# Kernel tuning notes

Measured on AMD Instinct MI355X. Metric: run time of the kernel, lower is better.

## Reference

```python
import jax, jax.numpy as jnp
import numpy as np
from jax import lax

HEADS = 8
WIN_SIZES = (2, 4, 8)


def _linear(x, w, b):
    return x @ w + b


def _window_attention(x2d, ws, w4, b4):
    # x2d: (B,H,W,C); w4: (4,C,C) = [q,k,v,out]; b4: (4,C)
    B, H, W, C = x2d.shape
    p1, p2 = H // ws, W // ws
    xw = x2d.reshape(B, p1, ws, p2, ws, C).transpose(0, 1, 3, 2, 4, 5)
    xw = xw.reshape(B, p1, p2, ws * ws, C)
    hs = C // HEADS
    q = _linear(xw, w4[0], b4[0]).reshape(B, p1, p2, ws * ws, HEADS, hs)
    k = _linear(xw, w4[1], b4[1]).reshape(B, p1, p2, ws * ws, HEADS, hs)
    v = _linear(xw, w4[2], b4[2]).reshape(B, p1, p2, ws * ws, HEADS, hs)
    scores = jnp.einsum('bpqwhd,bpqvhd->bpqhwv', q, k) / jnp.sqrt(jnp.asarray(hs, x2d.dtype))
    probs = jax.nn.softmax(scores, axis=-1)
    ctx = jnp.einsum('bpqhwv,bpqvhd->bpqwhd', probs, v).reshape(B, p1, p2, ws * ws, C)
    return _linear(ctx, w4[3], b4[3])


def _unwindow(out, ws):
    B, p1, p2, win, C = out.shape
    s = out.reshape(B, p1, p2, ws, ws, C).transpose(0, 1, 3, 2, 4, 5)
    return s.reshape(B, p1 * ws, p2 * ws, C)


def _up_bilinear_ac(x, oh, ow):
    # x: (B,C,h,w); bilinear with align_corners=True (UpsamplingBilinear2d)
    B, C, h, w = x.shape
    def grid(o, i):
        pos = jnp.arange(o, dtype=x.dtype) * ((i - 1) / (o - 1))
        i0 = jnp.floor(pos).astype(jnp.int32)
        i1 = jnp.minimum(i0 + 1, i - 1)
        return i0, i1, pos - i0.astype(x.dtype)
    r0, r1, tr = grid(oh, h)
    c0, c1, tc = grid(ow, w)
    xr = x[:, :, r0, :] * (1 - tr)[None, None, :, None] + x[:, :, r1, :] * tr[None, None, :, None]
    return xr[:, :, :, c0] * (1 - tc) + xr[:, :, :, c1] * tc


def _forward(x, attn_w, attn_b, edge_w, mlp_w1, mlp_b1, mlp_w2, mlp_b2,
             dl_w, dl_b, ax_w, ax_b, g_shift, g_bias, sq_w, sq_b):
    B, N, C = x.shape
    H = W = int(np.sqrt(N))
    x2d = x.reshape(B, H, W, C)

    # multi-scale window attention branches
    scale_outputs = [_unwindow(_window_attention(x2d, ws, attn_w[i], attn_b[i]), ws)
                     for i, ws in enumerate(WIN_SIZES)]

    # adaptive window selector
    xc = x2d.transpose(0, 3, 1, 2)  # (B,C,H,W)
    edge = jnp.abs(lax.conv_general_dilated(xc, edge_w, (1, 1), 'SAME'))
    avg = lax.reduce_window(edge, 0.0, lax.add, (1, 1, 3, 3), (1, 1, 1, 1), 'SAME') / 9.0
    e = avg.transpose(0, 2, 3, 1)  # (B,H,W,1)
    wts = jax.nn.softmax(jax.nn.relu(e @ mlp_w1 + mlp_b1) @ mlp_w2 + mlp_b2, axis=-1)

    blended = sum(wts[..., i:i + 1] * scale_outputs[i] for i in range(len(WIN_SIZES)))
    h_map = blended.transpose(0, 3, 1, 2)  # (B,C,H,W)

    # ws=4 window attention -> DlightConv token pooling
    x_win = _window_attention(x2d, 4, attn_w[1], attn_b[1])  # (B,p,p,16,C)
    probs = jax.nn.softmax(jnp.mean(x_win, axis=-2) @ dl_w + dl_b, axis=-1)
    x_dl = jnp.sum(x_win * probs[..., None], axis=-2)  # (B,p,p,C)

    # axial attention (no head split, no scaling in the axial branch)
    q = _linear(x_dl, ax_w[0], ax_b[0])
    k = _linear(x_dl, ax_w[1], ax_b[1])
    v = _linear(x_dl, ax_w[2], ax_b[2])
    scores_x = jnp.einsum('bhwc,bhvc->bhwv', q, k)  # (B,r,c,k)
    scores_y = jnp.einsum('bhwc,bvwc->bwhv', q, k)  # (B,c,r,k)

    # GaussianTrans: vectorized per-pixel gaussian positional bias
    p = x_dl.shape[1]
    idx = jnp.arange(p, dtype=x.dtype)
    dist2 = (idx[None, :] - idx[:, None]) ** 2          # [pos, k]
    gb = -(g_shift[0] * dist2 + g_bias[0])              # (p,p)
    ax = jax.nn.softmax(scores_x + gb[None, None, :, :], axis=-1)       # bias indexed by c
    ay = jax.nn.softmax(jnp.swapaxes(scores_y, 1, 2) + gb[None, :, None, :], axis=-1)  # bias by r
    x_g = jnp.einsum('brck,brkd->brcd', ax, v) + jnp.einsum('brck,bkcd->brcd', ay, v)

    x_g = _up_bilinear_ac(x_g.transpose(0, 3, 1, 2), H, W)  # (B,C,H,W)

    cat = jnp.concatenate([x_g, h_map], axis=1)  # (B,2C,H,W)
    out = jnp.einsum('oc,bchw->bohw', sq_w, cat) + sq_b[None, :, None, None]
    return out.transpose(0, 2, 3, 1).reshape(B, N, C)


def setup_inputs() -> dict:
    key = jax.random.key(0)
    ks = jax.random.split(key, 16)
    B, N, C = 16, 4096, 256
    s = 0.02
    return {
        'x': jax.random.normal(ks[0], (B, N, C), jnp.float32),
        'attn_w': jax.random.normal(ks[1], (3, 4, C, C), jnp.float32) * s,
        'attn_b': jax.random.normal(ks[2], (3, 4, C), jnp.float32) * s,
        'edge_w': jax.random.normal(ks[3], (1, C, 3, 3), jnp.float32) * s,
        'mlp_w1': jax.random.normal(ks[4], (1, 16), jnp.float32) * s,
        'mlp_b1': jax.random.normal(ks[5], (16,), jnp.float32) * s,
        'mlp_w2': jax.random.normal(ks[6], (16, 3), jnp.float32) * s,
        'mlp_b2': jax.random.normal(ks[7], (3,), jnp.float32) * s,
        'dl_w': jax.random.normal(ks[8], (C, 16), jnp.float32) * s,
        'dl_b': jax.random.normal(ks[9], (16,), jnp.float32) * s,
        'ax_w': jax.random.normal(ks[10], (3, C, C), jnp.float32) * s,
        'ax_b': jax.random.normal(ks[11], (3, C), jnp.float32) * s,
        'g_shift': jnp.abs(jax.random.normal(ks[12], (1,), jnp.float32)),
        'g_bias': -jnp.abs(jax.random.normal(ks[13], (1,), jnp.float32)),
        'sq_w': jax.random.normal(ks[14], (C, 2 * C), jnp.float32) * s,
        'sq_b': jax.random.normal(ks[15], (C,), jnp.float32) * s,
    }


def reference(x, attn_w, attn_b, edge_w, mlp_w1, mlp_b1, mlp_w2, mlp_b2,
              dl_w, dl_b, ax_w, ax_b, g_shift, g_bias, sq_w, sq_b):
    return _forward(x, attn_w, attn_b, edge_w, mlp_w1, mlp_b1, mlp_w2, mlp_b2,
                    dl_w, dl_b, ax_w, ax_b, g_shift, g_bias, sq_w, sq_b)
```

## Files before the change

kernel.cpp:

```cpp
#include <hip/hip_runtime.h>
#include <math.h>


#define CHUNK_B 4
#define CHUNK_TOK (CHUNK_B * 4096)
#define KS 32

typedef __attribute__((ext_vector_type(8))) short short8;
typedef __attribute__((ext_vector_type(8))) unsigned short ushort8;
typedef __attribute__((ext_vector_type(4))) float f32x4;

__device__ __forceinline__ ushort f2bf(float f) {
    union { float f; unsigned u; } v; v.f = f;
    unsigned r = v.u + 0x7fff + ((v.u >> 16) & 1);
    return (ushort)(r >> 16);
}
__device__ __forceinline__ float bf2f(ushort h) {
    union { unsigned u; float f; } v; v.u = ((unsigned)h) << 16; return v.f;
}
__device__ __forceinline__ void split2(float v, ushort& h, ushort& l) {
    h = f2bf(v);
    l = f2bf(v - bf2f(h));
}

__global__ __launch_bounds__(256) void split_w_kmajor(
    const float* __restrict__ W, ushort* __restrict__ Th, ushort* __restrict__ Tl, int nmats)
{
    const int idx = blockIdx.x * 256 + threadIdx.x;
    if (idx >= nmats * 65536) return;
    const int mat = idx >> 16, r = idx & 65535;
    const int n = r >> 8, k = r & 255;
    const float v = W[(size_t)mat * 65536 + k * 256 + n];
    ushort h, l; split2(v, h, l);
    Th[idx] = h; Tl[idx] = l;
}
__global__ __launch_bounds__(256) void split_w_nmajor(
    const float* __restrict__ W, ushort* __restrict__ Th, ushort* __restrict__ Tl, int total)
{
    const int idx = blockIdx.x * 256 + threadIdx.x;
    if (idx >= total) return;
    ushort h, l; split2(W[idx], h, l);
    Th[idx] = h; Tl[idx] = l;
}

__global__ __launch_bounds__(256) void split_x(
    const float* __restrict__ X, ushort* __restrict__ Xh, ushort* __restrict__ Xl)
{
    const size_t i4 = (size_t)blockIdx.x * 256 + threadIdx.x;
    const float4 v = *(const float4*)(X + i4 * 4);
    ushort4 h, l;
    split2(v.x, h.x, l.x); split2(v.y, h.y, l.y);
    split2(v.z, h.z, l.z); split2(v.w, h.w, l.w);
    *(ushort4*)(Xh + i4 * 4) = h;
    *(ushort4*)(Xl + i4 * 4) = l;
}

#define GEMM_DECLS                                                            \
    __shared__ ushort Ah[128 * KS], Al[128 * KS], Bh[128 * KS], Bl[128 * KS]; \
    const int tid = threadIdx.x;                                              \
    const int wave = tid >> 6, lane = tid & 63;                               \
    const int quad = lane >> 4, l16 = lane & 15;                              \
    const int wr = (wave >> 1) * 64, wc = (wave & 1) * 64;                    \
    f32x4 acc[4][4];                                                          \
    _Pragma("unroll") for (int i = 0; i < 4; i++)                             \
        _Pragma("unroll") for (int j = 0; j < 4; j++)                         \
            acc[i][j] = (f32x4){0.f, 0.f, 0.f, 0.f};

#define STAGE_US(dst, src, strideE, rowbase, k0e)                             \
    _Pragma("unroll") for (int cc = 0; cc < 2; cc++) {                        \
        const int ch = tid + cc * 256;                                        \
        const int r = ch >> 2, kc = (ch & 3) * 8;                             \
        *(ushort8*)&(dst)[ch * 8] =                                           \
            *(const ushort8*)((src) + (size_t)((rowbase) + r) * (strideE) + (k0e) + kc); \
    }

#define STAGE_F32(AhD, AlD, Aptr, kk)                                         \
    _Pragma("unroll") for (int cc = 0; cc < 2; cc++) {                        \
        const int ch = tid + cc * 256;                                        \
        const int r = ch >> 2, kc = (ch & 3) * 8;                             \
        const float* p = (Aptr) + (size_t)(m0 + r) * 256 + (kk) + kc;         \
        const float4 v0 = *(const float4*)p;                                  \
        const float4 v1 = *(const float4*)(p + 4);                            \
        ushort8 h, l; ushort hh, ll;                                          \
        split2(v0.x, hh, ll); h[0] = hh; l[0] = ll;                           \
        split2(v0.y, hh, ll); h[1] = hh; l[1] = ll;                           \
        split2(v0.z, hh, ll); h[2] = hh; l[2] = ll;                           \
        split2(v0.w, hh, ll); h[3] = hh; l[3] = ll;                           \
        split2(v1.x, hh, ll); h[4] = hh; l[4] = ll;                           \
        split2(v1.y, hh, ll); h[5] = hh; l[5] = ll;                           \
        split2(v1.z, hh, ll); h[6] = hh; l[6] = ll;                           \
        split2(v1.w, hh, ll); h[7] = hh; l[7] = ll;                           \
        *(ushort8*)&(AhD)[ch * 8] = h;                                        \
        *(ushort8*)&(AlD)[ch * 8] = l;                                        \
    }

#define GEMM_COMPUTE                                                          \
    {                                                                         \
        short8 afh[4], afl[4], bfh[4], bfl[4];                                \
        _Pragma("unroll") for (int i = 0; i < 4; i++) {                       \
            const int ro = (wr + i * 16 + l16) * KS + quad * 8;               \
            afh[i] = *(const short8*)&Ah[ro];                                 \
            afl[i] = *(const short8*)&Al[ro];                                 \
        }                                                                     \
        _Pragma("unroll") for (int j = 0; j < 4; j++) {                       \
            const int no = (wc + j * 16 + l16) * KS + quad * 8;               \
            bfh[j] = *(const short8*)&Bh[no];                                 \
            bfl[j] = *(const short8*)&Bl[no];                                 \
        }                                                                     \
        _Pragma("unroll") for (int i = 0; i < 4; i++)                         \
            _Pragma("unroll") for (int j = 0; j < 4; j++) {                   \
                acc[i][j] = __builtin_amdgcn_mfma_f32_16x16x32_bf16(          \
                    afh[i], bfh[j], acc[i][j], 0, 0, 0);                      \
                acc[i][j] = __builtin_amdgcn_mfma_f32_16x16x32_bf16(          \
                    afl[i], bfh[j], acc[i][j], 0, 0, 0);                      \
                acc[i][j] = __builtin_amdgcn_mfma_f32_16x16x32_bf16(          \
                    afh[i], bfl[j], acc[i][j], 0, 0, 0);                      \
            }                                                                 \
    }

__global__ __launch_bounds__(256, 2) void gemm3_mfma(
    const ushort* __restrict__ AgH, const ushort* __restrict__ AgL,
    const ushort* __restrict__ Wth, const ushort* __restrict__ Wtl,
    const float* __restrict__ b0, const float* __restrict__ b1, const float* __restrict__ b2,
    float* __restrict__ O0, float* __restrict__ O1, float* __restrict__ O2)
{
    const int m0 = blockIdx.x * 128;
    const int mat = blockIdx.y >> 1;
    const int col0 = (blockIdx.y & 1) * 128;
    const ushort* wth = Wth + (size_t)mat * 65536 + (size_t)col0 * 256;
    const ushort* wtl = Wtl + (size_t)mat * 65536 + (size_t)col0 * 256;
    GEMM_DECLS
    for (int k0 = 0; k0 < 256; k0 += 32) {
        STAGE_US(Ah, AgH, 256, m0, k0)
        STAGE_US(Al, AgL, 256, m0, k0)
        STAGE_US(Bh, wth, 256, 0, k0)
        STAGE_US(Bl, wtl, 256, 0, k0)
        __syncthreads();
        GEMM_COMPUTE
        __syncthreads();
    }
    const float* bias = (mat == 0) ? b0 : (mat == 1) ? b1 : b2;
    float* O = (mat == 0) ? O0 : (mat == 1) ? O1 : O2;
#pragma unroll
    for (int j = 0; j < 4; j++) {
        const int col = col0 + wc + j * 16 + l16;
        const float bj = bias[col];
#pragma unroll
        for (int i = 0; i < 4; i++) {
            const int rbase = m0 + wr + i * 16 + quad * 4;
#pragma unroll
            for (int r = 0; r < 4; r++)
                O[(size_t)(rbase + r) * 256 + col] = acc[i][j][r] + bj;
        }
    }
}

__global__ __launch_bounds__(256, 2) void gemmp_mfma(
    const ushort* __restrict__ AgH, const ushort* __restrict__ AgL,
    const ushort* __restrict__ Wth, const ushort* __restrict__ Wtl,
    const float* __restrict__ bias,
    float* __restrict__ Sout, int store_s,
    float* __restrict__ Blnd, const float* __restrict__ wts, int scale_idx, int blend_init,
    int row_off)
{
    const int m0 = blockIdx.x * 128;
    const int col0 = blockIdx.y * 128;
    const ushort* wth = Wth + (size_t)col0 * 256;
    const ushort* wtl = Wtl + (size_t)col0 * 256;
    GEMM_DECLS
    for (int k0 = 0; k0 < 256; k0 += 32) {
        STAGE_US(Ah, AgH, 256, m0, k0)
        STAGE_US(Al, AgL, 256, m0, k0)
        STAGE_US(Bh, wth, 256, 0, k0)
        STAGE_US(Bl, wtl, 256, 0, k0)
        __syncthreads();
        GEMM_COMPUTE
        __syncthreads();
    }
#pragma unroll
    for (int i = 0; i < 4; i++) {
        const int rbase = m0 + wr + i * 16 + quad * 4;
#pragma unroll
        for (int r = 0; r < 4; r++) {
            const size_t grow = (size_t)row_off + rbase + r;
            const float wt = wts[grow * 3 + scale_idx];
#pragma unroll
            for (int j = 0; j < 4; j++) {
                const int col = col0 + wc + j * 16 + l16;
                const float v = acc[i][j][r] + bias[col];
                if (store_s) Sout[grow * 256 + col] = v;
                float* bp = Blnd + grow * 256 + col;
                if (blend_init) *bp = wt * v;
                else            *bp = *bp + wt * v;
            }
        }
    }
}

__global__ __launch_bounds__(256, 2) void gemmf_mfma(
    const ushort* __restrict__ UPH, const ushort* __restrict__ UPL,
    const float* __restrict__ BLD,
    const ushort* __restrict__ Wth, const ushort* __restrict__ Wtl,
    const float* __restrict__ SQB, float* __restrict__ OUT)
{
    const int m0 = blockIdx.x * 128;
    const int col0 = blockIdx.y * 128;
    const ushort* wth = Wth + (size_t)col0 * 512;
    const ushort* wtl = Wtl + (size_t)col0 * 512;
    GEMM_DECLS
    for (int k0 = 0; k0 < 512; k0 += 32) {
        if (k0 < 256) {
            STAGE_US(Ah, UPH, 256, m0, k0)
            STAGE_US(Al, UPL, 256, m0, k0)
        } else {
            STAGE_F32(Ah, Al, BLD, (k0 & 255))
        }
        STAGE_US(Bh, wth, 512, 0, k0)
        STAGE_US(Bl, wtl, 512, 0, k0)
        __syncthreads();
        GEMM_COMPUTE
        __syncthreads();
    }
#pragma unroll
    for (int j = 0; j < 4; j++) {
        const int col = col0 + wc + j * 16 + l16;
        const float bj = SQB[col];
#pragma unroll
        for (int i = 0; i < 4; i++) {
            const int rbase = m0 + wr + i * 16 + quad * 4;
#pragma unroll
            for (int r = 0; r < 4; r++)
                OUT[(size_t)(rbase + r) * 256 + col] = acc[i][j][r] + bj;
        }
    }
}

template <int WS, int NH>
__global__ __launch_bounds__(256) void win_attn(
    const float* __restrict__ Q, const float* __restrict__ K,
    const float* __restrict__ V, ushort* __restrict__ CTXh, ushort* __restrict__ CTXl)
{
    constexpr int WIN = WS * WS;
    constexpr int NW = 64 / WS;
    constexpr int CW = NH * 32;
    __shared__ float qs[WIN][CW + 4], ks[WIN][CW + 4], vs[WIN][CW + 4];
    __shared__ float sc[NH][WIN][WIN + 1];
    const int tid = threadIdx.x;
    const int wid = blockIdx.x;
    const int b = wid / (NW * NW);
    const int rem = wid % (NW * NW);
    const int p = rem / NW, q = rem % NW;
    const int h0 = blockIdx.y * NH;

    for (int idx = tid; idx < WIN * CW; idx += 256) {
        const int i = idx / CW;
        const int cc = idx % CW;
        const int ti = i / WS, tj = i % WS;
        const size_t g = ((size_t)(b * 4096 + (p * WS + ti) * 64 + (q * WS + tj))) * 256 + h0 * 32 + cc;
        qs[i][cc] = Q[g]; ks[i][cc] = K[g]; vs[i][cc] = V[g];
    }
    __syncthreads();
    const float scale = 0.17677669529663687f;
    for (int idx = tid; idx < NH * WIN * WIN; idx += 256) {
        const int hl = idx / (WIN * WIN);
        const int r = idx % (WIN * WIN);
        const int i = r / WIN, j = r % WIN;
        const int co = hl * 32;
        float s = 0.f;
#pragma unroll
        for (int d = 0; d < 32; d++) s += qs[i][co + d] * ks[j][co + d];
        sc[hl][i][j] = s * scale;
    }
    __syncthreads();
    if (tid < NH * WIN) {
        const int hl = tid / WIN, i = tid % WIN;
        float mx = -3.4e38f;
        for (int j = 0; j < WIN; j++) mx = fmaxf(mx, sc[hl][i][j]);
        float sum = 0.f;
        for (int j = 0; j < WIN; j++) {
            float e = __expf(sc[hl][i][j] - mx);
            sc[hl][i][j] = e; sum += e;
        }
        const float inv = 1.f / sum;
        for (int j = 0; j < WIN; j++) sc[hl][i][j] *= inv;
    }
    __syncthreads();
    for (int idx = tid; idx < WIN * CW; idx += 256) {
        const int i = idx / CW;
        const int cc = idx % CW;
        const int hl = cc >> 5;
        float s = 0.f;
        for (int j = 0; j < WIN; j++) s += sc[hl][i][j] * vs[j][cc];
        const int ti = i / WS, tj = i % WS;
        const size_t g = ((size_t)(b * 4096 + (p * WS + ti) * 64 + (q * WS + tj))) * 256 + h0 * 32 + cc;
        ushort hh, ll; split2(s, hh, ll);
        CTXh[g] = hh; CTXl[g] = ll;
    }
}

__global__ __launch_bounds__(256) void edge_gemm9(
    const float* __restrict__ x, const float* __restrict__ ew, float* __restrict__ ytmp)
{
    __shared__ float wsm[2304];
    const int tid = threadIdx.x;
    for (int i = tid; i < 2304; i += 256) wsm[i] = ew[i];
    __syncthreads();
    const int wave = tid >> 6, lane = tid & 63;
    const int p = blockIdx.x * 4 + wave;
    const float4 xv = *(const float4*)(x + (size_t)p * 256 + lane * 4);
    float acc[9];
#pragma unroll
    for (int t = 0; t < 9; t++) acc[t] = 0.f;
    const float xs[4] = {xv.x, xv.y, xv.z, xv.w};
#pragma unroll
    for (int i = 0; i < 4; i++) {
        const int c = lane * 4 + i;
#pragma unroll
        for (int t = 0; t < 9; t++)
            acc[t] = fmaf(xs[i], wsm[c * 9 + t], acc[t]);
    }
#pragma unroll
    for (int t = 0; t < 9; t++) {
#pragma unroll
        for (int off = 1; off < 64; off <<= 1)
            acc[t] += __shfl_xor(acc[t], off);
    }
    if (lane < 9) {
        float v = acc[0];
        switch (lane) {
            case 1: v = acc[1]; break; case 2: v = acc[2]; break;
            case 3: v = acc[3]; break; case 4: v = acc[4]; break;
            case 5: v = acc[5]; break; case 6: v = acc[6]; break;
            case 7: v = acc[7]; break; case 8: v = acc[8]; break;
            default: break;
        }
        ytmp[(size_t)p * 9 + lane] = v;
    }
}

__global__ __launch_bounds__(256) void edge_combine(
    const float* __restrict__ ytmp, float* __restrict__ edge)
{
    const int idx = blockIdx.x * 256 + threadIdx.x;
    const int b = idx >> 12, rem = idx & 4095, h = rem >> 6, w = rem & 63;
    float s = 0.f;
#pragma unroll
    for (int kh = 0; kh < 3; kh++) {
        const int hh = h + kh - 1;
        if ((unsigned)hh > 63u) continue;
#pragma unroll
        for (int kw = 0; kw < 3; kw++) {
            const int ww = w + kw - 1;
            if ((unsigned)ww > 63u) continue;
            s += ytmp[((size_t)b * 4096 + hh * 64 + ww) * 9 + kh * 3 + kw];
        }
    }
    edge[idx] = fabsf(s);
}

__global__ __launch_bounds__(256) void avg_mlp(
    const float* __restrict__ edge, const float* __restrict__ w1, const float* __restrict__ b1,
    const float* __restrict__ w2, const float* __restrict__ b2, float* __restrict__ wts)
{
    const int idx = blockIdx.x * 256 + threadIdx.x;
    const int b = idx >> 12, rem = idx & 4095, h = rem >> 6, w = rem & 63;
    float s = 0.f;
#pragma unroll
    for (int kh = -1; kh <= 1; kh++) {
        const int hh = h + kh;
        if ((unsigned)hh > 63u) continue;
#pragma unroll
        for (int kw = -1; kw <= 1; kw++) {
            const int ww = w + kw;
            if ((unsigned)ww > 63u) continue;
            s += edge[(size_t)b * 4096 + hh * 64 + ww];
        }
    }
    const float e = s / 9.f;
    float l0 = b2[0], l1 = b2[1], l2 = b2[2];
#pragma unroll
    for (int j = 0; j < 16; j++) {
        float hd = fmaxf(e * w1[j] + b1[j], 0.f);
        l0 += hd * w2[j * 3 + 0];
        l1 += hd * w2[j * 3 + 1];
        l2 += hd * w2[j * 3 + 2];
    }
    const float mx = fmaxf(l0, fmaxf(l1, l2));
    const float e0 = __expf(l0 - mx), e1 = __expf(l1 - mx), e2 = __expf(l2 - mx);
    const float inv = 1.f / (e0 + e1 + e2);
    wts[(size_t)idx * 3 + 0] = e0 * inv;
    wts[(size_t)idx * 3 + 1] = e1 * inv;
    wts[(size_t)idx * 3 + 2] = e2 * inv;
}

__global__ __launch_bounds__(256) void dlight(
    const float* __restrict__ S1, const float* __restrict__ dlw,
    const float* __restrict__ dlb, ushort* __restrict__ XDLH, ushort* __restrict__ XDLL)
{
    __shared__ float xw[16][257];
    __shared__ float m[256];
    __shared__ float pr[16];
    __shared__ float pr2[16];
    const int wid = blockIdx.x;
    const int b = wid >> 8, rem = wid & 255, p = rem >> 4, q = rem & 15;
    const int tid = threadIdx.x;
#pragma unroll
    for (int t = 0; t < 16; t++) {
        const int ti = t >> 2, tj = t & 3;
        xw[t][tid] = S1[((size_t)b * 4096 + (p * 4 + ti) * 64 + (q * 4 + tj)) * 256 + tid];
    }
    float mm = 0.f;
#pragma unroll
    for (int t = 0; t < 16; t++) mm += xw[t][tid];
    m[tid] = mm * (1.f / 16.f);
    __syncthreads();
    if (tid < 16) {
        float lg = dlb[tid];
        for (int c = 0; c < 256; c++) lg += m[c] * dlw[c * 16 + tid];
        pr[tid] = lg;
    }
    __syncthreads();
    if (tid < 16) {
        float mx = -3.4e38f;
        for (int j = 0; j < 16; j++) mx = fmaxf(mx, pr[j]);
        float sum = 0.f;
        for (int j = 0; j < 16; j++) sum += __expf(pr[j] - mx);
        pr2[tid] = __expf(pr[tid] - mx) / sum;
    }
    __syncthreads();
    float o = 0.f;
#pragma unroll
    for (int t = 0; t < 16; t++) o += xw[t][tid] * pr2[t];
    ushort hh, ll; split2(o, hh, ll);
    XDLH[(size_t)wid * 256 + tid] = hh;
    XDLL[(size_t)wid * 256 + tid] = ll;
}

__global__ __launch_bounds__(256) void axial_row(
    const float* __restrict__ Q, const float* __restrict__ K, const float* __restrict__ V,
    const float* __restrict__ gsp, const float* __restrict__ gbp, float* __restrict__ XG)
{
    __shared__ float qs[16][257], ks[16][257], vs[16][257];
    __shared__ float sc[16][17];
    const int bid = blockIdx.x;
    const int b = bid >> 4, r = bid & 15;
    const int tid = threadIdx.x;
    const float gs = gsp[0], gb = gbp[0];
#pragma unroll
    for (int w = 0; w < 16; w++) {
        const size_t base = ((size_t)b * 256 + r * 16 + w) * 256 + tid;
        qs[w][tid] = Q[base]; ks[w][tid] = K[base]; vs[w][tid] = V[base];
    }
    __syncthreads();
    {
        const int w = tid >> 4, vv = tid & 15;
        float s = 0.f;
        for (int c = 0; c < 256; c++) s += qs[w][c] * ks[vv][c];
        const float d = (float)(w - vv);
        sc[w][vv] = s - (gs * d * d + gb);
    }
    __syncthreads();
    if (tid < 16) {
        float mx = -3.4e38f;
        for (int j = 0; j < 16; j++) mx = fmaxf(mx, sc[tid][j]);
        float sum = 0.f;
        for (int j = 0; j < 16; j++) {
            float e = __expf(sc[tid][j] - mx);
            sc[tid][j] = e; sum += e;
        }
        const float inv = 1.f / sum;
        for (int j = 0; j < 16; j++) sc[tid][j] *= inv;
    }
    __syncthreads();
#pragma unroll
    for (int w2 = 0; w2 < 16; w2++) {
        float o = 0.f;
#pragma unroll
        for (int k2 = 0; k2 < 16; k2++) o += sc[w2][k2] * vs[k2][tid];
        XG[((size_t)b * 256 + r * 16 + w2) * 256 + tid] = o;
    }
}

__global__ __launch_bounds__(256) void axial_col(
    const float* __restrict__ Q, const float* __restrict__ K, const float* __restrict__ V,
    const float* __restrict__ gsp, const float* __restrict__ gbp, float* __restrict__ XG)
{
    __shared__ float qs[16][257], ks[16][257], vs[16][257];
    __shared__ float sc[16][17];
    const int bid = blockIdx.x;
    const int b = bid >> 4, col = bid & 15;
    const int tid = threadIdx.x;
    const float gs = gsp[0], gb = gbp[0];
#pragma unroll
    for (int h = 0; h < 16; h++) {
        const size_t base = ((size_t)b * 256 + h * 16 + col) * 256 + tid;
        qs[h][tid] = Q[base]; ks[h][tid] = K[base]; vs[h][tid] = V[base];
    }
    __syncthreads();
    {
        const int r = tid >> 4, vv = tid & 15;
        float s = 0.f;
        for (int c = 0; c < 256; c++) s += qs[r][c] * ks[vv][c];
        const float d = (float)(r - vv);
        sc[r][vv] = s - (gs * d * d + gb);
    }
    __syncthreads();
    if (tid < 16) {
        float mx = -3.4e38f;
        for (int j = 0; j < 16; j++) mx = fmaxf(mx, sc[tid][j]);
        float sum = 0.f;
        for (int j = 0; j < 16; j++) {
            float e = __expf(sc[tid][j] - mx);
            sc[tid][j] = e; sum += e;
        }
        const float inv = 1.f / sum;
        for (int j = 0; j < 16; j++) sc[tid][j] *= inv;
    }
    __syncthreads();
#pragma unroll
    for (int r2 = 0; r2 < 16; r2++) {
        float o = 0.f;
#pragma unroll
        for (int k2 = 0; k2 < 16; k2++) o += sc[r2][k2] * vs[k2][tid];
        XG[((size_t)b * 256 + r2 * 16 + col) * 256 + tid] += o;
    }
}

__global__ __launch_bounds__(256) void upsample(
    const float* __restrict__ XG, ushort* __restrict__ UPH, ushort* __restrict__ UPL)
{
    const unsigned idx = blockIdx.x * 256u + threadIdx.x;
    const int c = idx & 255;
    const unsigned t2 = idx >> 8;
    const int w = t2 & 63;
    const unsigned t3 = t2 >> 6;
    const int h = t3 & 63;
    const int b = t3 >> 6;
    const float rr = 15.f / 63.f;
    const float ph = h * rr, pw = w * rr;
    int h0 = (int)floorf(ph); float th = ph - (float)h0; int h1 = min(h0 + 1, 15);
    int w0 = (int)floorf(pw); float tw = pw - (float)w0; int w1 = min(w0 + 1, 15);
    const size_t bb = (size_t)b * 256;
    const float v00 = XG[((bb + h0 * 16 + w0)) * 256 + c];
    const float v10 = XG[((bb + h1 * 16 + w0)) * 256 + c];
    const float v01 = XG[((bb + h0 * 16 + w1)) * 256 + c];
    const float v11 = XG[((bb + h1 * 16 + w1)) * 256 + c];
    const float c0 = v00 * (1.f - th) + v10 * th;
    const float c1 = v01 * (1.f - th) + v11 * th;
    const float val = c0 * (1.f - tw) + c1 * tw;
    ushort hh, ll; split2(val, hh, ll);
    UPH[idx] = hh; UPL[idx] = ll;
}

extern "C" void kernel_launch(void* const* d_in, const int* in_sizes, int n_in,
                              void* d_out, int out_size, void* d_ws, size_t ws_size,
                              hipStream_t stream)
{
    const float* x      = (const float*)d_in[0];
    const float* attn_w = (const float*)d_in[1];
    const float* attn_b = (const float*)d_in[2];
    const float* edge_w = (const float*)d_in[3];
    const float* mlp_w1 = (const float*)d_in[4];
    const float* mlp_b1 = (const float*)d_in[5];
    const float* mlp_w2 = (const float*)d_in[6];
    const float* mlp_b2 = (const float*)d_in[7];
    const float* dl_w   = (const float*)d_in[8];
    const float* dl_b   = (const float*)d_in[9];
    const float* ax_w   = (const float*)d_in[10];
    const float* ax_b   = (const float*)d_in[11];
    const float* g_shift= (const float*)d_in[12];
    const float* g_bias = (const float*)d_in[13];
    const float* sq_w   = (const float*)d_in[14];
    const float* sq_b   = (const float*)d_in[15];
    float* out = (float*)d_out;

    float* ws = (float*)d_ws;
    const size_t MT = 65536;
    float* blend = ws;
    float* s1    = blend + MT * 256;
    float* scr   = s1 + MT * 256;
    float* chQ   = scr;
    float* chK   = chQ + (size_t)CHUNK_TOK * 256;
    float* chV   = chK + (size_t)CHUNK_TOK * 256;
    ushort* ctxh = (ushort*)(chV + (size_t)CHUNK_TOK * 256);
    ushort* ctxl = ctxh + (size_t)CHUNK_TOK * 256;
    ushort* uph  = (ushort*)scr;
    ushort* upl  = uph + MT * 256;
    float* ytmp  = scr;
    float* edge  = scr + MT * 256;
    float* wts   = edge + 65536;
    float* xdl   = wts + 196608;
    ushort* xdlh = (ushort*)xdl;
    ushort* xdll = xdlh + 1048576;
    float* axq   = xdl + 1048576;
    float* axk   = axq + 1048576;
    float* axv   = axk + 1048576;
    float* xg    = axv + 1048576;
    ushort* Wth = (ushort*)(xg + 1048576);
    ushort* Wtl = Wth + 1114112;
    ushort* xh = (ushort*)out;
    ushort* xl = xh + MT * 256;

    split_w_kmajor<<<(12 * 65536 + 255) / 256, 256, 0, stream>>>(attn_w, Wth, Wtl, 12);
    split_w_kmajor<<<(3 * 65536 + 255) / 256, 256, 0, stream>>>(
        ax_w, Wth + (size_t)12 * 65536, Wtl + (size_t)12 * 65536, 3);
    split_w_nmajor<<<(131072 + 255) / 256, 256, 0, stream>>>(
        sq_w, Wth + (size_t)15 * 65536, Wtl + (size_t)15 * 65536, 131072);

    split_x<<<16384, 256, 0, stream>>>(x, xh, xl);

    edge_gemm9<<<16384, 256, 0, stream>>>(x, edge_w, ytmp);
    edge_combine<<<256, 256, 0, stream>>>(ytmp, edge);
    avg_mlp<<<256, 256, 0, stream>>>(edge, mlp_w1, mlp_b1, mlp_w2, mlp_b2, wts);

    for (int i = 0; i < 3; i++) {
        const ushort* Wh = Wth + (size_t)i * 4 * 65536;
        const ushort* Wl = Wtl + (size_t)i * 4 * 65536;
        const float* c0 = attn_b + (size_t)(i * 4 + 0) * 256;
        const float* c1 = attn_b + (size_t)(i * 4 + 1) * 256;
        const float* c2 = attn_b + (size_t)(i * 4 + 2) * 256;
        const float* c3 = attn_b + (size_t)(i * 4 + 3) * 256;
        for (int ch = 0; ch < 16 / CHUNK_B; ch++) {
            const size_t toff = (size_t)ch * CHUNK_TOK;
            gemm3_mfma<<<dim3(CHUNK_TOK / 128, 6), 256, 0, stream>>>(
                xh + toff * 256, xl + toff * 256, Wh, Wl, c0, c1, c2, chQ, chK, chV);
            if (i == 0)
                win_attn<2, 8><<<dim3(CHUNK_B * 32 * 32, 1), 256, 0, stream>>>(chQ, chK, chV, ctxh, ctxl);
            if (i == 1)
                win_attn<4, 4><<<dim3(CHUNK_B * 16 * 16, 2), 256, 0, stream>>>(chQ, chK, chV, ctxh, ctxl);
            if (i == 2)
                win_attn<8, 1><<<dim3(CHUNK_B * 8 * 8, 8), 256, 0, stream>>>(chQ, chK, chV, ctxh, ctxl);
            gemmp_mfma<<<dim3(CHUNK_TOK / 128, 2), 256, 0, stream>>>(
                ctxh, ctxl, Wh + (size_t)3 * 65536, Wl + (size_t)3 * 65536, c3,
                s1, (i == 1) ? 1 : 0, blend, wts, i, (i == 0) ? 1 : 0, (int)toff);
        }
    }

    dlight<<<4096, 256, 0, stream>>>(s1, dl_w, dl_b, xdlh, xdll);

    gemm3_mfma<<<dim3(4096 / 128, 6), 256, 0, stream>>>(
        xdlh, xdll, Wth + (size_t)12 * 65536, Wtl + (size_t)12 * 65536,
        ax_b, ax_b + 256, ax_b + 512, axq, axk, axv);
    axial_row<<<256, 256, 0, stream>>>(axq, axk, axv, g_shift, g_bias, xg);
    axial_col<<<256, 256, 0, stream>>>(axq, axk, axv, g_shift, g_bias, xg);

    upsample<<<65536, 256, 0, stream>>>(xg, uph, upl);

    gemmf_mfma<<<dim3(512, 2), 256, 0, stream>>>(
        uph, upl, blend, Wth + (size_t)15 * 65536, Wtl + (size_t)15 * 65536, sq_b, out);
}
```

Before: 1.361 ms.

## Stage GEMM tiles via global_load_lds with XOR swizzle; fuse x split into edge kernel

GEMM tile staging now uses direct global-to-LDS loads (global_load_lds, 16 bytes) instead of loading through registers and then storing to LDS. The LDS layout gets an XOR swizzle on the k-quarter index to reduce bank conflicts on the MFMA fragment reads. The F32 staging path and the fragment loads are updated to match. Separately, the bf16 hi/lo split of x is folded into edge_gemm9, which removes one launch and a second full read of x. The swizzle must agree exactly between the writers and the readers, which is a correctness risk.

```diff
diff --git a/kernel.cpp b/kernel.cpp
--- a/kernel.cpp
+++ b/kernel.cpp
@@ -21,6 +21,13 @@
 __device__ __forceinline__ void split2(float v, ushort& h, ushort& l) {
     h = f2bf(v);
     l = f2bf(v - bf2f(h));
+}
+
+__device__ __forceinline__ void gld16(const ushort* g, ushort* l) {
+    __builtin_amdgcn_global_load_lds(
+        (const __attribute__((address_space(1))) unsigned int*)g,
+        (__attribute__((address_space(3))) unsigned int*)l,
+        16, 0, 0);
 }
 
 __global__ __launch_bounds__(256) void split_w_kmajor(
@@ -41,18 +48,6 @@
     if (idx >= total) return;
     ushort h, l; split2(W[idx], h, l);
     Th[idx] = h; Tl[idx] = l;
-}
-
-__global__ __launch_bounds__(256) void split_x(
-    const float* __restrict__ X, ushort* __restrict__ Xh, ushort* __restrict__ Xl)
-{
-    const size_t i4 = (size_t)blockIdx.x * 256 + threadIdx.x;
-    const float4 v = *(const float4*)(X + i4 * 4);
-    ushort4 h, l;
-    split2(v.x, h.x, l.x); split2(v.y, h.y, l.y);
-    split2(v.z, h.z, l.z); split2(v.w, h.w, l.w);
-    *(ushort4*)(Xh + i4 * 4) = h;
-    *(ushort4*)(Xl + i4 * 4) = l;
 }
 
 #define GEMM_DECLS                                                            \
@@ -66,19 +61,20 @@
         _Pragma("unroll") for (int j = 0; j < 4; j++)                         \
             acc[i][j] = (f32x4){0.f, 0.f, 0.f, 0.f};
 
-#define STAGE_US(dst, src, strideE, rowbase, k0e)                             \
-    _Pragma("unroll") for (int cc = 0; cc < 2; cc++) {                        \
-        const int ch = tid + cc * 256;                                        \
-        const int r = ch >> 2, kc = (ch & 3) * 8;                             \
-        *(ushort8*)&(dst)[ch * 8] =                                           \
-            *(const ushort8*)((src) + (size_t)((rowbase) + r) * (strideE) + (k0e) + kc); \
+#define STAGE_GLD(dstbuf, srcp, strideE, rowbase, k0e)                        \
+    _Pragma("unroll") for (int jj = 0; jj < 2; jj++) {                        \
+        const int rr = (wave << 5) + (jj << 4) + (lane >> 2);                 \
+        const int kqs = (lane & 3) ^ ((lane >> 3) & 3);                       \
+        gld16((srcp) + (size_t)((rowbase) + rr) * (strideE) + (k0e) + (kqs << 3), \
+              (dstbuf) + (wave << 10) + (jj << 9));                           \
     }
 
 #define STAGE_F32(AhD, AlD, Aptr, kk)                                         \
     _Pragma("unroll") for (int cc = 0; cc < 2; cc++) {                        \
         const int ch = tid + cc * 256;                                        \
-        const int r = ch >> 2, kc = (ch & 3) * 8;                             \
-        const float* p = (Aptr) + (size_t)(m0 + r) * 256 + (kk) + kc;         \
+        const int r = ch >> 2, kq = ch & 3;                                   \
+        const int wsl = (kq ^ ((r >> 1) & 3)) * 8;                            \
+        const float* p = (Aptr) + (size_t)(m0 + r) * 256 + (kk) + kq * 8;     \
         const float4 v0 = *(const float4*)p;                                  \
         const float4 v1 = *(const float4*)(p + 4);                            \
         ushort8 h, l; ushort hh, ll;                                          \
@@ -90,20 +86,21 @@
         split2(v1.y, hh, ll); h[5] = hh; l[5] = ll;                           \
         split2(v1.z, hh, ll); h[6] = hh; l[6] = ll;                           \
         split2(v1.w, hh, ll); h[7] = hh; l[7] = ll;                           \
-        *(ushort8*)&(AhD)[ch * 8] = h;                                        \
-        *(ushort8*)&(AlD)[ch * 8] = l;                                        \
+        *(ushort8*)&(AhD)[r * KS + wsl] = h;                                  \
+        *(ushort8*)&(AlD)[r * KS + wsl] = l;                                  \
     }
 
 #define GEMM_COMPUTE                                                          \
     {                                                                         \
+        const int aswz = (l16 & 6) << 2;                  \
         short8 afh[4], afl[4], bfh[4], bfl[4];                                \
         _Pragma("unroll") for (int i = 0; i < 4; i++) {                       \
-            const int ro = (wr + i * 16 + l16) * KS + quad * 8;               \
+            const int ro = (wr + i * 16 + l16) * KS + ((quad * 8) ^ aswz);    \
             afh[i] = *(const short8*)&Ah[ro];                                 \
             afl[i] = *(const short8*)&Al[ro];                                 \
         }                                                                     \
         _Pragma("unroll") for (int j = 0; j < 4; j++) {                       \
-            const int no = (wc + j * 16 + l16) * KS + quad * 8;               \
+            const int no = (wc + j * 16 + l16) * KS + ((quad * 8) ^ aswz);    \
             bfh[j] = *(const short8*)&Bh[no];                                 \
             bfl[j] = *(const short8*)&Bl[no];                                 \
         }                                                                     \
@@ -131,10 +128,10 @@
     const ushort* wtl = Wtl + (size_t)mat * 65536 + (size_t)col0 * 256;
     GEMM_DECLS
     for (int k0 = 0; k0 < 256; k0 += 32) {
-        STAGE_US(Ah, AgH, 256, m0, k0)
-        STAGE_US(Al, AgL, 256, m0, k0)
-        STAGE_US(Bh, wth, 256, 0, k0)
-        STAGE_US(Bl, wtl, 256, 0, k0)
+        STAGE_GLD(Ah, AgH, 256, m0, k0)
+        STAGE_GLD(Al, AgL, 256, m0, k0)
+        STAGE_GLD(Bh, wth, 256, 0, k0)
+        STAGE_GLD(Bl, wtl, 256, 0, k0)
         __syncthreads();
         GEMM_COMPUTE
         __syncthreads();
@@ -169,10 +166,10 @@
     const ushort* wtl = Wtl + (size_t)col0 * 256;
     GEMM_DECLS
     for (int k0 = 0; k0 < 256; k0 += 32) {
-        STAGE_US(Ah, AgH, 256, m0, k0)
-        STAGE_US(Al, AgL, 256, m0, k0)
-        STAGE_US(Bh, wth, 256, 0, k0)
-        STAGE_US(Bl, wtl, 256, 0, k0)
+        STAGE_GLD(Ah, AgH, 256, m0, k0)
+        STAGE_GLD(Al, AgL, 256, m0, k0)
+        STAGE_GLD(Bh, wth, 256, 0, k0)
+        STAGE_GLD(Bl, wtl, 256, 0, k0)
         __syncthreads();
         GEMM_COMPUTE
         __syncthreads();
@@ -210,13 +207,13 @@
     GEMM_DECLS
     for (int k0 = 0; k0 < 512; k0 += 32) {
         if (k0 < 256) {
-            STAGE_US(Ah, UPH, 256, m0, k0)
-            STAGE_US(Al, UPL, 256, m0, k0)
+            STAGE_GLD(Ah, UPH, 256, m0, k0)
+            STAGE_GLD(Al, UPL, 256, m0, k0)
         } else {
             STAGE_F32(Ah, Al, BLD, (k0 & 255))
         }
-        STAGE_US(Bh, wth, 512, 0, k0)
-        STAGE_US(Bl, wtl, 512, 0, k0)
+        STAGE_GLD(Bh, wth, 512, 0, k0)
+        STAGE_GLD(Bl, wtl, 512, 0, k0)
         __syncthreads();
         GEMM_COMPUTE
         __syncthreads();
@@ -299,7 +296,8 @@
 }
 
 __global__ __launch_bounds__(256) void edge_gemm9(
-    const float* __restrict__ x, const float* __restrict__ ew, float* __restrict__ ytmp)
+    const float* __restrict__ x, const float* __restrict__ ew, float* __restrict__ ytmp,
+    ushort* __restrict__ Xh, ushort* __restrict__ Xl)
 {
     __shared__ float wsm[2304];
     const int tid = threadIdx.x;
@@ -308,6 +306,13 @@
     const int wave = tid >> 6, lane = tid & 63;
     const int p = blockIdx.x * 4 + wave;
     const float4 xv = *(const float4*)(x + (size_t)p * 256 + lane * 4);
+    {
+        ushort4 h4, l4;
+        split2(xv.x, h4.x, l4.x); split2(xv.y, h4.y, l4.y);
+        split2(xv.z, h4.z, l4.z); split2(xv.w, h4.w, l4.w);
+        *(ushort4*)(Xh + (size_t)p * 256 + lane * 4) = h4;
+        *(ushort4*)(Xl + (size_t)p * 256 + lane * 4) = l4;
+    }
     float acc[9];
 #pragma unroll
     for (int t = 0; t < 9; t++) acc[t] = 0.f;
@@ -607,9 +612,7 @@
     split_w_nmajor<<<(131072 + 255) / 256, 256, 0, stream>>>(
         sq_w, Wth + (size_t)15 * 65536, Wtl + (size_t)15 * 65536, 131072);
 
-    split_x<<<16384, 256, 0, stream>>>(x, xh, xl);
-
-    edge_gemm9<<<16384, 256, 0, stream>>>(x, edge_w, ytmp);
+    edge_gemm9<<<16384, 256, 0, stream>>>(x, edge_w, ytmp, xh, xl);
     edge_combine<<<256, 256, 0, stream>>>(ytmp, edge);
     avg_mlp<<<256, 256, 0, stream>>>(edge, mlp_w1, mlp_b1, mlp_w2, mlp_b2, wts);
 
```

New measurement: 1.300 ms. 1.05x faster.
